# Kernel optimization log

Hardware: AMD Instinct MI355X
Metric: run time of the kernel (lower is better)

## Reference

```python
import jax, jax.numpy as jnp
import numpy as np
from jax import lax

B, T, C = 8, 1025, 512
HEADS = 8
CACHE = 256          # int(dim * cache_ratio)
CLS = 1
L = 256              # gr_cache memory length
H = W = 32           # sqrt(T - CLS)
EPS = 1e-5


def setup_inputs() -> dict:
    key = jax.random.key(0)
    ks = jax.random.split(key, 40)
    def w(k, shape, scale=0.02):
        return jax.random.normal(k, shape, dtype=jnp.float32) * scale
    inp = {}
    inp['x'] = jax.random.normal(ks[0], (B, T, C), dtype=jnp.float32)
    inp['gr_cache'] = jax.random.normal(ks[1], (1, L, CACHE), dtype=jnp.float32)
    # self-attention (dim=512) params, weights stored (in, out)
    inp['Wq1'] = w(ks[2], (C, C)); inp['bq1'] = jnp.zeros((C,), jnp.float32)
    inp['Wk1'] = w(ks[3], (C, C)); inp['bk1'] = jnp.zeros((C,), jnp.float32)
    inp['Wv1'] = w(ks[4], (C, C)); inp['bv1'] = jnp.zeros((C,), jnp.float32)
    inp['Wo1'] = w(ks[5], (C, C)); inp['bo1'] = jnp.zeros((C,), jnp.float32)
    # memory attention (dim=cache_dim=256) params
    inp['Wq2'] = w(ks[6], (CACHE, CACHE)); inp['bq2'] = jnp.zeros((CACHE,), jnp.float32)
    inp['Wk2'] = w(ks[7], (CACHE, CACHE)); inp['bk2'] = jnp.zeros((CACHE,), jnp.float32)
    inp['Wv2'] = w(ks[8], (CACHE, CACHE)); inp['bv2'] = jnp.zeros((CACHE,), jnp.float32)
    inp['Wo2'] = w(ks[9], (CACHE, CACHE)); inp['bo2'] = jnp.zeros((CACHE,), jnp.float32)
    # GRU-style gate linears: in = 2*cache_dim, out = cache_dim
    inp['Wr'] = w(ks[10], (2 * CACHE, CACHE)); inp['br'] = jnp.zeros((CACHE,), jnp.float32)
    inp['Wz'] = w(ks[11], (2 * CACHE, CACHE)); inp['bz'] = jnp.zeros((CACHE,), jnp.float32)
    inp['Wa'] = w(ks[12], (2 * CACHE, CACHE)); inp['ba'] = jnp.zeros((CACHE,), jnp.float32)
    # LayerNorm(cache_dim)
    inp['gamma'] = jnp.ones((CACHE,), jnp.float32)
    inp['beta'] = jnp.zeros((CACHE,), jnp.float32)
    # per-head gate logits, init to -1 as in the module
    inp['lam'] = jnp.full((HEADS,), -1.0, dtype=jnp.float32)
    # grouped conv pos-emb: Conv2d(512, 512, k=3, groups=CACHE) -> (O=512, I/g=2, 3, 3)
    inp['conv_w'] = w(ks[13], (C, C // CACHE, 3, 3))
    inp['conv_b'] = jnp.zeros((C,), jnp.float32)
    return inp


def _mha(q_in, kv_in, Wq, bq, Wk, bk, Wv, bv, Wo, bo):
    Bq, Tq, D = q_in.shape
    Tk = kv_in.shape[1]
    dh = D // HEADS
    q = (q_in @ Wq + bq).reshape(Bq, Tq, HEADS, dh)
    k = (kv_in @ Wk + bk).reshape(Bq, Tk, HEADS, dh)
    v = (kv_in @ Wv + bv).reshape(Bq, Tk, HEADS, dh)
    s = jnp.einsum('bqhd,bkhd->bhqk', q, k) * (1.0 / np.sqrt(dh)).astype(np.float32)
    a = jax.nn.softmax(s, axis=-1)
    o = jnp.einsum('bhqk,bkhd->bqhd', a, v).reshape(Bq, Tq, D)
    return o @ Wo + bo


def reference(x, gr_cache, Wq1, bq1, Wk1, bk1, Wv1, bv1, Wo1, bo1,
              Wq2, bq2, Wk2, bk2, Wv2, bv2, Wo2, bo2,
              Wr, br, Wz, bz, Wa, ba, gamma, beta, lam, conv_w, conv_b):
    B_, T_, C_ = x.shape
    # ---- spatial positional embedding (faithful to torch view->permute quirk) ----
    tok = x[:, CLS:, :].reshape(B_, H, W, C_).transpose(0, 3, 1, 2)   # (B, C, H, W)
    pos = lax.conv_general_dilated(tok, conv_w, (1, 1), 'SAME',
                                   feature_group_count=CACHE,
                                   dimension_numbers=('NCHW', 'OIHW', 'NCHW'))
    pos = pos + conv_b[None, :, None, None]
    pos = pos.reshape(B_, C_, T_ - CLS).transpose(0, 2, 1)            # (B, T-1, C)
    pos = jnp.concatenate([jnp.zeros((B_, CLS, C_), pos.dtype), pos], axis=1)
    # ---- self attention ----
    x_self = _mha(x, x, Wq1, bq1, Wk1, bk1, Wv1, bv1, Wo1, bo1)       # (B, T, C)
    x_self_h = x_self.reshape(B_, T_, HEADS, C_ // HEADS)
    # ---- GRU-style gated cache update ----
    gr = jnp.broadcast_to(gr_cache, (B_, L, CACHE))
    x_summary = x_self[:, :, :CACHE]
    idx = (jnp.arange(L) * T_) // L                                   # nearest interpolate T -> L
    x_summary = x_summary[:, idx, :]                                  # (B, L, CACHE)
    cat = jnp.concatenate([gr, x_summary], axis=-1)
    reset = jax.nn.sigmoid(cat @ Wr + br)
    z = jax.nn.sigmoid(cat @ Wz + bz)
    cat2 = jnp.concatenate([reset * gr, x_summary], axis=-1)
    add = jax.nn.gelu(cat2 @ Wa + ba, approximate=False)
    mu = add.mean(-1, keepdims=True)
    var = ((add - mu) ** 2).mean(-1, keepdims=True)
    add = (add - mu) / jnp.sqrt(var + EPS) * gamma + beta             # LayerNorm
    gr_new = z * add + (1.0 - z) * gr
    # ---- memory attention on first cache_dim channels ----
    x_mem = _mha(x[:, :, :CACHE], gr_new, Wq2, bq2, Wk2, bk2, Wv2, bv2, Wo2, bo2)
    x_mem = x_mem.reshape(B_, T_, HEADS, CACHE // HEADS)
    # ---- per-head alpha blend with zero-padded mem branch ----
    alpha = jax.nn.sigmoid(lam).reshape(1, 1, HEADS, 1)
    pad = jnp.zeros((B_, T_, HEADS, (C_ - CACHE) // HEADS), x.dtype)
    out = (alpha * jnp.concatenate([x_mem, pad], axis=-1)
           + (1.0 - alpha) * x_self_h).reshape(B_, T_, C_) + pos
    return out
```

## Files before the change

kernel.cpp:

```cpp
#include <hip/hip_runtime.h>
#include <math.h>

typedef unsigned short u16;
typedef unsigned int u32;
typedef __attribute__((ext_vector_type(8))) short short8;
typedef __attribute__((ext_vector_type(4))) short short4v;
typedef __attribute__((ext_vector_type(4))) float f32x4;

constexpr int Bc = 8;
constexpr int Tt = 1025;
constexpr int Cc = 512;
constexpr int Hn = 8;
constexpr int CA = 256;
constexpr int Ll = 256;

#if __has_builtin(__builtin_amdgcn_exp2f)
#define EXP2F __builtin_amdgcn_exp2f
#else
#define EXP2F exp2f
#endif

__device__ __forceinline__ u16 f2bf(float f) {
  u32 u = __builtin_bit_cast(u32, f);
  u = (u + 0x7FFFu + ((u >> 16) & 1u)) >> 16;
  return (u16)u;
}
__device__ __forceinline__ u32 pack2f(float lo, float hi) {
  const u32 a = __builtin_bit_cast(u32, hi) + 0x8000u;
  const u32 b = __builtin_bit_cast(u32, lo) + 0x8000u;
  return __builtin_amdgcn_perm(a, b, 0x07060302u);
}

struct WC { const float* s; u16* d; int sN; int sK; int kshift; int tot; };
struct WCP { WC w[11]; };

__global__ void wcast_k(WCP p) {
  const WC a = p.w[blockIdx.y];
  const int kmask = (1 << a.kshift) - 1;
  for (int idx = blockIdx.x * 256 + threadIdx.x; idx < a.tot; idx += gridDim.x * 256) {
    const int k = idx & kmask;
    const int n = idx >> a.kshift;
    a.d[idx] = (k < a.sK) ? f2bf(a.s[(size_t)k * a.sN + n]) : (u16)0;
  }
}

enum { EP_NONE = 0, EP_SIGMOID = 1, EP_GELU = 2 };

struct GemmEpi {
  const float* bias[4];
  int start[4];
  float scale[4];
  int nreg;
};

template <int AF32, int OUTBF, int ACT>
__global__ __launch_bounds__(256) void gemm_mfma(
    const void* __restrict__ Av, int lda,
    const u16* __restrict__ Wt,
    GemmEpi epi,
    void* __restrict__ Cout,
    int M, int N, int K)
{
  __shared__ u16 As[128][32];
  __shared__ u16 Bs[128][32];
  const int tid = threadIdx.x;
  const int m0 = blockIdx.y * 128, n0 = blockIdx.x * 128;
  const int ln = tid & 15, quad = (tid >> 4) & 3, wv = tid >> 6;
  const int wm = (wv & 1) * 64, wn = (wv >> 1) * 64;
  const int sr = tid >> 1;
  const int sk = (tid & 1) * 16;

  f32x4 zf = {0.f, 0.f, 0.f, 0.f};
  f32x4 acc[4][4];
  #pragma unroll
  for (int i = 0; i < 4; i++)
    #pragma unroll
    for (int j = 0; j < 4; j++) acc[i][j] = zf;

  const short8 z8 = {0, 0, 0, 0, 0, 0, 0, 0};

  for (int k0 = 0; k0 < K; k0 += 32) {
    const int gm = m0 + sr;
    short8 a0 = z8, a1 = z8;
    if (gm < M) {
      if (AF32) {
        const float* p = (const float*)Av + (size_t)gm * lda + k0 + sk;
        const float4 f0 = *(const float4*)(p + 0);
        const float4 f1 = *(const float4*)(p + 4);
        const float4 f2 = *(const float4*)(p + 8);
        const float4 f3 = *(const float4*)(p + 12);
        ((u32*)&a0)[0] = pack2f(f0.x, f0.y);
        ((u32*)&a0)[1] = pack2f(f0.z, f0.w);
        ((u32*)&a0)[2] = pack2f(f1.x, f1.y);
        ((u32*)&a0)[3] = pack2f(f1.z, f1.w);
        ((u32*)&a1)[0] = pack2f(f2.x, f2.y);
        ((u32*)&a1)[1] = pack2f(f2.z, f2.w);
        ((u32*)&a1)[2] = pack2f(f3.x, f3.y);
        ((u32*)&a1)[3] = pack2f(f3.z, f3.w);
      } else {
        const u16* p = (const u16*)Av + (size_t)gm * lda + k0 + sk;
        a0 = *(const short8*)p;
        a1 = *(const short8*)(p + 8);
      }
    }
    *(short8*)&As[sr][sk] = a0;
    *(short8*)&As[sr][sk + 8] = a1;
    {
      const u16* q = Wt + (size_t)(n0 + sr) * K + k0 + sk;
      *(short8*)&Bs[sr][sk] = *(const short8*)q;
      *(short8*)&Bs[sr][sk + 8] = *(const short8*)(q + 8);
    }
    __syncthreads();

    short8 af[4], bf[4];
    #pragma unroll
    for (int i = 0; i < 4; i++) af[i] = *(const short8*)&As[wm + i * 16 + ln][quad * 8];
    #pragma unroll
    for (int j = 0; j < 4; j++) bf[j] = *(const short8*)&Bs[wn + j * 16 + ln][quad * 8];
    #pragma unroll
    for (int i = 0; i < 4; i++)
      #pragma unroll
      for (int j = 0; j < 4; j++)
        acc[i][j] = __builtin_amdgcn_mfma_f32_16x16x32_bf16(af[i], bf[j], acc[i][j], 0, 0, 0);
    __syncthreads();
  }

  int ri = 0;
  #pragma unroll
  for (int i = 1; i < 4; i++)
    if (i < epi.nreg && epi.start[i] <= n0) ri = i;
  const float* bp = epi.bias[ri] - epi.start[ri];
  const float sc = epi.scale[ri];

  float bj[4];
  #pragma unroll
  for (int j = 0; j < 4; j++) bj[j] = bp[n0 + wn + j * 16 + ln];

  #pragma unroll
  for (int i = 0; i < 4; i++) {
    #pragma unroll
    for (int r = 0; r < 4; r++) {
      const int gm = m0 + wm + i * 16 + quad * 4 + r;
      if (gm >= M) continue;
      #pragma unroll
      for (int j = 0; j < 4; j++) {
        float v = (acc[i][j][r] + bj[j]) * sc;
        if (ACT == EP_SIGMOID)   v = 1.f / (1.f + __expf(-v));
        else if (ACT == EP_GELU) v = 0.5f * v * (1.f + erff(v * 0.70710678118654752f));
        const size_t off = (size_t)gm * N + n0 + wn + j * 16 + ln;
        if (OUTBF) ((u16*)Cout)[off] = f2bf(v);
        else       ((float*)Cout)[off] = v;
      }
    }
  }
}

template <int DH>
__global__ __launch_bounds__(128) void attn_mfma(
    const u16* __restrict__ Qp, const u16* __restrict__ Kp,
    const u16* __restrict__ Vp, u16* __restrict__ Op,
    int Tq, int Tk, int qbs, int kbs, int obs, int qrs, int krs, int ors)
{
  constexpr int NC = DH / 32;
  constexpr int NM = DH / 16;

  __shared__ u16 Vt[2][DH * 32];
  __shared__ u16 Pb[2 * 32 * 32];

  const int b = blockIdx.y >> 3, h = blockIdx.y & 7;
  const int q0 = blockIdx.x * 64;
  const int tid = threadIdx.x;
  const int wv = tid >> 6;
  const int lane = tid & 63;
  const int ln = lane & 15, quad = lane >> 4;

  const u16* Qb = Qp + (size_t)b * qbs + h * DH;
  const u16* Kb = Kp + (size_t)b * kbs + h * DH;
  const u16* Vb = Vp + (size_t)b * kbs + h * DH;
  u16* Ob = Op + (size_t)b * obs + h * DH;

  const short8 z8 = {0, 0, 0, 0, 0, 0, 0, 0};
  const f32x4 zf = {0.f, 0.f, 0.f, 0.f};

  short8 qf[2][NC];
  #pragma unroll
  for (int qs = 0; qs < 2; qs++) {
    const int gq = q0 + wv * 32 + qs * 16 + ln;
    #pragma unroll
    for (int c = 0; c < NC; c++) {
      if (gq < Tq) qf[qs][c] = *(const short8*)(Qb + (size_t)gq * qrs + c * 32 + quad * 8);
      else         qf[qs][c] = z8;
    }
  }

  f32x4 oacc[2][NM];
  float lsum[2] = {0.f, 0.f};
  #pragma unroll
  for (int qs = 0; qs < 2; qs++)
    #pragma unroll
    for (int c = 0; c < NM; c++) oacc[qs][c] = zf;

  const int vd0 = (tid & 15) * (DH / 16);
  const int vk = (tid >> 4) * 4;
  const int gb = vk >> 3, off = vk & 7;

  const int nfull = Tk >> 5;
  const int nit = (Tk + 31) >> 5;
  const int tkm1 = Tk - 1;

  auto loadK = [&](int it, short8 (&kf)[2][NC]) {
    #pragma unroll
    for (int kc = 0; kc < 2; kc++)
      #pragma unroll
      for (int c = 0; c < NC; c++) {
        int row = (it << 5) + kc * 16 + ln;
        row = row < tkm1 ? row : tkm1;
        kf[kc][c] = *(const short8*)(Kb + (size_t)row * krs + c * 32 + quad * 8);
      }
  };
  auto loadV = [&](int it, short4v (&vr)[4]) {
    #pragma unroll
    for (int i2 = 0; i2 < 4; i2++) {
      int gk = (it << 5) + vk + i2;
      gk = gk < tkm1 ? gk : tkm1;
      short4v t = {0, 0, 0, 0};
      if (DH == 64) {
        t = *(const short4v*)(Vb + (size_t)gk * krs + vd0);
      } else {
        ushort2 u = *(const ushort2*)(Vb + (size_t)gk * krs + vd0);
        t[0] = (short)u.x; t[1] = (short)u.y;
      }
      vr[i2] = t;
    }
  };

  auto body = [&](int it, short8 (&kfC)[2][NC], short4v (&vrC)[4],
                  short8 (&kfN)[2][NC], short4v (&vrN)[4]) {
    const bool full = (it < nfull);
    u16* vt = &Vt[it & 1][0];
    const int k0 = it << 5;

    #pragma unroll
    for (int i = 0; i < DH / 16; i++) {
      const int d = vd0 + i;
      const int h2 = (d ^ (d >> 3)) & 3;
      short4v w = {vrC[0][i], vrC[1][i], vrC[2][i], vrC[3][i]};
      *(short4v*)&vt[d * 32 + ((gb ^ h2) << 3) + off] = w;
    }
    if (it + 1 < nit) { loadK(it + 1, kfN); loadV(it + 1, vrN); }
    __syncthreads();

    #pragma unroll
    for (int qs = 0; qs < 2; qs++) {
      #pragma unroll
      for (int kc = 0; kc < 2; kc++) {
        f32x4 s = zf;
        #pragma unroll
        for (int c = 0; c < NC; c++)
          s = __builtin_amdgcn_mfma_f32_16x16x32_bf16(kfC[kc][c], qf[qs][c], s, 0, 0, 0);
        float p0, p1, p2, p3;
        if (full) {
          p0 = EXP2F(s[0]); p1 = EXP2F(s[1]); p2 = EXP2F(s[2]); p3 = EXP2F(s[3]);
        } else {
          const int kb = k0 + kc * 16 + quad * 4;
          p0 = (kb + 0 < Tk) ? EXP2F(s[0]) : 0.f;
          p1 = (kb + 1 < Tk) ? EXP2F(s[1]) : 0.f;
          p2 = (kb + 2 < Tk) ? EXP2F(s[2]) : 0.f;
          p3 = (kb + 3 < Tk) ? EXP2F(s[3]) : 0.f;
        }
        lsum[qs] += (p0 + p1) + (p2 + p3);
        short4v pw;
        ((u32*)&pw)[0] = pack2f(p0, p1);
        ((u32*)&pw)[1] = pack2f(p2, p3);
        const int q = qs * 16 + ln;
        const int g = ((kc * 2 + (quad >> 1)) ^ (ln & 3)) & 3;
        *(short4v*)&Pb[wv * 1024 + q * 32 + (g << 3) + (quad & 1) * 4] = pw;
      }
    }

    short8 pf2[2];
    #pragma unroll
    for (int qs = 0; qs < 2; qs++) {
      const int q = qs * 16 + ln;
      const int g = quad ^ (ln & 3);
      pf2[qs] = *(const short8*)&Pb[wv * 1024 + q * 32 + g * 8];
    }
    #pragma unroll
    for (int c = 0; c < NM; c++) {
      const int d = c * 16 + ln;
      const int g = quad ^ ((d ^ (d >> 3)) & 3);
      const short8 vf = *(const short8*)&vt[d * 32 + g * 8];
      #pragma unroll
      for (int qs = 0; qs < 2; qs++)
        oacc[qs][c] = __builtin_amdgcn_mfma_f32_16x16x32_bf16(pf2[qs], vf, oacc[qs][c], 0, 0, 0);
    }
  };

  short8 kfA[2][NC], kfB[2][NC];
  short4v vrA[4], vrB[4];
  loadK(0, kfA);
  loadV(0, vrA);

  int it = 0;
  for (; it + 1 < nit; it += 2) {
    body(it, kfA, vrA, kfB, vrB);
    body(it + 1, kfB, vrB, kfA, vrA);
  }
  if (it < nit) body(it, kfA, vrA, kfB, vrB);

  float lq[2];
  #pragma unroll
  for (int qs = 0; qs < 2; qs++) {
    float t = lsum[qs];
    t += __shfl_xor(t, 16);
    t += __shfl_xor(t, 32);
    lq[qs] = t;
  }
  #pragma unroll
  for (int qs = 0; qs < 2; qs++) {
    #pragma unroll
    for (int r = 0; r < 4; r++) {
      const float linv = 1.f / __shfl(lq[qs], quad * 4 + r);
      const int gq = q0 + wv * 32 + qs * 16 + quad * 4 + r;
      if (gq >= Tq) continue;
      #pragma unroll
      for (int c = 0; c < NM; c++)
        Ob[(size_t)gq * ors + c * 16 + ln] = f2bf(oacc[qs][c][r] * linv);
    }
  }
}

__global__ __launch_bounds__(256) void conv_combine(
    const float* __restrict__ x, const float* __restrict__ cw,
    const float* __restrict__ cb, const float* __restrict__ x_self,
    const float* __restrict__ x_mem, const float* __restrict__ lam,
    float* __restrict__ out)
{
  const int bh = blockIdx.x;
  const int b = bh >> 5, hh = bh & 31;
  const int c = (blockIdx.y << 8) + threadIdx.x;
  const int ci = c & ~1;
  const int dd = c & 63;
  const int h8 = c >> 6;
  const float alpha = 1.f / (1.f + __expf(-lam[h8]));
  const float bias = cb[c];

  float wgt[2][9];
  #pragma unroll
  for (int ch = 0; ch < 2; ch++)
    #pragma unroll
    for (int k = 0; k < 9; k++) wgt[ch][k] = cw[c * 18 + ch * 9 + k];

  const float* xrow[3];
  bool rv[3];
  #pragma unroll
  for (int r = 0; r < 3; r++) {
    const int h2 = hh + r - 1;
    rv[r] = (unsigned)h2 < 32u;
    xrow[r] = x + ((size_t)(b * Tt) + 1 + h2 * 32) * Cc + ci;
  }

  float2 win[3][3];
  #pragma unroll
  for (int r = 0; r < 3; r++) {
    win[r][0] = make_float2(0.f, 0.f);
    win[r][1] = rv[r] ? *(const float2*)(xrow[r]) : make_float2(0.f, 0.f);
  }

  const size_t bT = (size_t)b * Tt;
  for (int w = 0; w < 32; w++) {
    #pragma unroll
    for (int r = 0; r < 3; r++)
      win[r][2] = (rv[r] && w + 1 < 32) ? *(const float2*)(xrow[r] + (w + 1) * Cc)
                                        : make_float2(0.f, 0.f);
    float pos = bias;
    #pragma unroll
    for (int r = 0; r < 3; r++)
      #pragma unroll
      for (int col = 0; col < 3; col++) {
        pos += win[r][col].x * wgt[0][r * 3 + col];
        pos += win[r][col].y * wgt[1][r * 3 + col];
      }
    const size_t bt = bT + 1 + hh * 32 + w;
    const float mem = (dd < 32) ? x_mem[bt * 256 + h8 * 32 + dd] : 0.f;
    out[bt * 512 + c] = pos + alpha * mem + (1.f - alpha) * x_self[bt * 512 + c];
    #pragma unroll
    for (int r = 0; r < 3; r++) { win[r][0] = win[r][1]; win[r][1] = win[r][2]; }
  }

  if (hh == 0) {
    const float mem = (dd < 32) ? x_mem[bT * 256 + h8 * 32 + dd] : 0.f;
    out[bT * 512 + c] = alpha * mem + (1.f - alpha) * x_self[bT * 512 + c];
  }
}

__global__ void build_cat(const float* __restrict__ gr_cache,
                          const float* __restrict__ x_self,
                          u16* __restrict__ cat)
{
  const int idx = blockIdx.x * 256 + threadIdx.x;
  if (idx >= Bc * Ll * 512) return;
  const int k = idx & 511;
  const int bi = idx >> 9;
  const int i = bi & 255;
  const int b = bi >> 8;
  float v;
  if (k < 256) v = gr_cache[i * 256 + k];
  else         v = x_self[((size_t)(b * Tt + 4 * i)) * Cc + (k - 256)];
  cat[idx] = f2bf(v);
}

__global__ void build_cat2(const float* __restrict__ gr_cache,
                           const float* __restrict__ rzg,
                           u16* __restrict__ cat)
{
  const int idx = blockIdx.x * 256 + threadIdx.x;
  if (idx >= Bc * Ll * 256) return;
  const int k = idx & 255;
  const int bi = idx >> 8;
  const int i = bi & 255;
  cat[(size_t)bi * 512 + k] = f2bf(gr_cache[i * 256 + k] * rzg[(size_t)bi * 512 + k]);
}

__device__ inline float block_sum256(float v, float* red)
{
  #pragma unroll
  for (int o = 32; o >= 1; o >>= 1) v += __shfl_down(v, o);
  const int wid = threadIdx.x >> 6;
  if ((threadIdx.x & 63) == 0) red[wid] = v;
  __syncthreads();
  const float t = red[0] + red[1] + red[2] + red[3];
  __syncthreads();
  return t;
}

__global__ __launch_bounds__(256) void ln_gate(
    const float* __restrict__ add_raw, const float* __restrict__ rzg,
    const float* __restrict__ gr_cache, const float* __restrict__ gamma,
    const float* __restrict__ beta, u16* __restrict__ gr_new)
{
  __shared__ float red[4];
  const int bi = blockIdx.x;
  const int i = bi & 255;
  const int c = threadIdx.x;
  const float v = add_raw[(size_t)bi * 256 + c];
  const float mu = block_sum256(v, red) * (1.f / 256.f);
  const float dv = v - mu;
  const float var = block_sum256(dv * dv, red) * (1.f / 256.f);
  const float nrm = dv * rsqrtf(var + 1e-5f) * gamma[c] + beta[c];
  const float zz = rzg[(size_t)bi * 512 + 256 + c];
  gr_new[(size_t)bi * 256 + c] = f2bf(zz * nrm + (1.f - zz) * gr_cache[i * 256 + c]);
}

extern "C" void kernel_launch(void* const* d_in, const int* in_sizes, int n_in,
                              void* d_out, int out_size, void* d_ws, size_t ws_size,
                              hipStream_t stream)
{
  const float* x        = (const float*)d_in[0];
  const float* gr_cache = (const float*)d_in[1];
  const float* Wq1 = (const float*)d_in[2];  const float* bq1 = (const float*)d_in[3];
  const float* Wk1 = (const float*)d_in[4];  const float* bk1 = (const float*)d_in[5];
  const float* Wv1 = (const float*)d_in[6];  const float* bv1 = (const float*)d_in[7];
  const float* Wo1 = (const float*)d_in[8];  const float* bo1 = (const float*)d_in[9];
  const float* Wq2 = (const float*)d_in[10]; const float* bq2 = (const float*)d_in[11];
  const float* Wk2 = (const float*)d_in[12]; const float* bk2 = (const float*)d_in[13];
  const float* Wv2 = (const float*)d_in[14]; const float* bv2 = (const float*)d_in[15];
  const float* Wo2 = (const float*)d_in[16]; const float* bo2 = (const float*)d_in[17];
  const float* Wr  = (const float*)d_in[18]; const float* br  = (const float*)d_in[19];
  const float* Wz  = (const float*)d_in[20]; const float* bz  = (const float*)d_in[21];
  const float* Wa  = (const float*)d_in[22]; const float* ba  = (const float*)d_in[23];
  const float* gamma = (const float*)d_in[24];
  const float* beta  = (const float*)d_in[25];
  const float* lam   = (const float*)d_in[26];
  const float* conv_w = (const float*)d_in[27];
  const float* conv_b = (const float*)d_in[28];
  float* out = (float*)d_out;

  const int M1 = Bc * Tt;
  const int M2 = Bc * Ll;
  const size_t BLA = (size_t)Bc * Ll * CA;
  const size_t BL2 = (size_t)Bc * Ll * 512;

  char* W = (char*)d_ws;
  u16*   qkvq  = (u16*)(W + 0);
  u16*   att1  = (u16*)(W + 29388800);
  u16*   att2  = (u16*)(W + 29388800);
  float* x_self= (float*)(W + 37785600);
  u16*   cat   = (u16*)(W + 54579200);
  float* rzg   = (float*)(W + 56676352);
  float* addr_ = (float*)(W + 60870656);
  float* x_mem = (float*)(W + 54579200);
  u16*   gr_new= (u16*)(W + 62976000);
  u16*   k2v2  = (u16*)(W + 64024576);
  u16*   wtb   = (u16*)(W + 66121728);

  u16* megaW = wtb;
  u16* o1W   = wtb + 917504;
  u16* rzW   = wtb + 1179648;
  u16* aW    = wtb + 1441792;
  u16* kvW   = wtb + 1572864;
  u16* o2W   = wtb + 1703936;

  const dim3 blk(256);

  {
    WCP p;
    p.w[0]  = {Wq1, megaW + 0,           512, 512, 9, 512 * 512};
    p.w[1]  = {Wk1, megaW + 512 * 512,   512, 512, 9, 512 * 512};
    p.w[2]  = {Wv1, megaW + 1024 * 512,  512, 512, 9, 512 * 512};
    p.w[3]  = {Wq2, megaW + 1536 * 512,  256, 256, 9, 256 * 512};
    p.w[4]  = {Wo1, o1W,                 512, 512, 9, 512 * 512};
    p.w[5]  = {Wr,  rzW + 0,             256, 512, 9, 256 * 512};
    p.w[6]  = {Wz,  rzW + 256 * 512,     256, 512, 9, 256 * 512};
    p.w[7]  = {Wa,  aW,                  256, 512, 9, 256 * 512};
    p.w[8]  = {Wk2, kvW + 0,             256, 256, 8, 256 * 256};
    p.w[9]  = {Wv2, kvW + 256 * 256,     256, 256, 8, 256 * 256};
    p.w[10] = {Wo2, o2W,                 256, 256, 8, 256 * 256};
    wcast_k<<<dim3(64, 11), blk, 0, stream>>>(p);
  }

  const float sQ1 = 0.18033688011112042f;
  const float sQ2 = 0.25503490664918414f;

  {
    GemmEpi e;
    e.bias[0] = bq1; e.start[0] = 0;    e.scale[0] = sQ1;
    e.bias[1] = bk1; e.start[1] = 512;  e.scale[1] = 1.f;
    e.bias[2] = bv1; e.start[2] = 1024; e.scale[2] = 1.f;
    e.bias[3] = bq2; e.start[3] = 1536; e.scale[3] = sQ2;
    e.nreg = 4;
    gemm_mfma<1, 1, EP_NONE><<<dim3(14, 65), blk, 0, stream>>>(
        x, 512, megaW, e, qkvq, M1, 1792, 512);
  }

  attn_mfma<64><<<dim3(17, 64), dim3(128), 0, stream>>>(
      qkvq, qkvq + 512, qkvq + 1024, att1, Tt, Tt,
      Tt * 1792, Tt * 1792, Tt * 512, 1792, 1792, 512);

  {
    GemmEpi e; e.bias[0] = bo1; e.start[0] = 0; e.scale[0] = 1.f; e.nreg = 1;
    gemm_mfma<0, 0, EP_NONE><<<dim3(4, 65), blk, 0, stream>>>(
        att1, 512, o1W, e, x_self, M1, 512, 512);
  }

  build_cat<<<(int)((BL2 + 255) / 256), blk, 0, stream>>>(gr_cache, x_self, cat);
  {
    GemmEpi e;
    e.bias[0] = br; e.start[0] = 0;   e.scale[0] = 1.f;
    e.bias[1] = bz; e.start[1] = 256; e.scale[1] = 1.f;
    e.nreg = 2;
    gemm_mfma<0, 0, EP_SIGMOID><<<dim3(4, 16), blk, 0, stream>>>(
        cat, 512, rzW, e, rzg, M2, 512, 512);
  }
  build_cat2<<<(int)((BLA + 255) / 256), blk, 0, stream>>>(gr_cache, rzg, cat);
  {
    GemmEpi e; e.bias[0] = ba; e.start[0] = 0; e.scale[0] = 1.f; e.nreg = 1;
    gemm_mfma<0, 0, EP_GELU><<<dim3(2, 16), blk, 0, stream>>>(
        cat, 512, aW, e, addr_, M2, 256, 512);
  }
  ln_gate<<<M2, blk, 0, stream>>>(addr_, rzg, gr_cache, gamma, beta, gr_new);

  {
    GemmEpi e;
    e.bias[0] = bk2; e.start[0] = 0;   e.scale[0] = 1.f;
    e.bias[1] = bv2; e.start[1] = 256; e.scale[1] = 1.f;
    e.nreg = 2;
    gemm_mfma<0, 1, EP_NONE><<<dim3(4, 16), blk, 0, stream>>>(
        gr_new, 256, kvW, e, k2v2, M2, 512, 256);
  }

  attn_mfma<32><<<dim3(17, 64), dim3(128), 0, stream>>>(
      qkvq + 1536, k2v2, k2v2 + 256, att2, Tt, Ll,
      Tt * 1792, Ll * 512, Tt * 256, 1792, 512, 256);

  {
    GemmEpi e; e.bias[0] = bo2; e.start[0] = 0; e.scale[0] = 1.f; e.nreg = 1;
    gemm_mfma<0, 0, EP_NONE><<<dim3(2, 65), blk, 0, stream>>>(
        att2, 256, o2W, e, x_mem, M1, 256, 256);
  }

  conv_combine<<<dim3(Bc * 32, 2), blk, 0, stream>>>(x, conv_w, conv_b, x_self,
                                                     x_mem, lam, out);
}
```

Measured before the change: 370.4 us.

## Split attention key range across two wave pairs and combine in LDS

The attention kernel now launches 256 threads per block. Two pairs of waves each process half of the key/value iterations for the same 64 queries, then reduce their partial output accumulators and row sums through shared memory before normalising. This doubles the waves available per block to hide memory and MFMA latency, given the modest block count. The cost is extra LDS for per-pair V tiles, a combine step with two barriers, and block-wide barriers now shared by both pairs.

```diff
diff --git a/kernel.cpp b/kernel.cpp
--- a/kernel.cpp
+++ b/kernel.cpp
@@ -156,23 +156,31 @@
 }
 
 template <int DH>
-__global__ __launch_bounds__(128) void attn_mfma(
+__global__ __launch_bounds__(256) void attn_mfma(
     const u16* __restrict__ Qp, const u16* __restrict__ Kp,
     const u16* __restrict__ Vp, u16* __restrict__ Op,
     int Tq, int Tk, int qbs, int kbs, int obs, int qrs, int krs, int ors)
 {
   constexpr int NC = DH / 32;
   constexpr int NM = DH / 16;
-
-  __shared__ u16 Vt[2][DH * 32];
-  __shared__ u16 Pb[2 * 32 * 32];
+  constexpr int VTE = 2 * DH * 32;
+  constexpr int PAY = 2 * NM * 4 + 2;
+  constexpr int PSTR = PAY | 1;
+
+  __shared__ __align__(16) char smem[2 * VTE * 2 + 4 * 1024 * 2];
+  static_assert(128 * PSTR * 4 <= 2 * VTE * 2 + 4 * 1024 * 2, "combine fits");
+  u16* const VtP = (u16*)smem;
+  u16* const PbP = (u16*)(smem + 2 * VTE * 2);
 
   const int b = blockIdx.y >> 3, h = blockIdx.y & 7;
   const int q0 = blockIdx.x * 64;
   const int tid = threadIdx.x;
   const int wv = tid >> 6;
+  const int pair = wv >> 1;
+  const int wvp = wv & 1;
   const int lane = tid & 63;
   const int ln = lane & 15, quad = lane >> 4;
+  const int lt = tid & 127;
 
   const u16* Qb = Qp + (size_t)b * qbs + h * DH;
   const u16* Kb = Kp + (size_t)b * kbs + h * DH;
@@ -185,7 +193,7 @@
   short8 qf[2][NC];
   #pragma unroll
   for (int qs = 0; qs < 2; qs++) {
-    const int gq = q0 + wv * 32 + qs * 16 + ln;
+    const int gq = q0 + wvp * 32 + qs * 16 + ln;
     #pragma unroll
     for (int c = 0; c < NC; c++) {
       if (gq < Tq) qf[qs][c] = *(const short8*)(Qb + (size_t)gq * qrs + c * 32 + quad * 8);
@@ -200,13 +208,16 @@
     #pragma unroll
     for (int c = 0; c < NM; c++) oacc[qs][c] = zf;
 
-  const int vd0 = (tid & 15) * (DH / 16);
-  const int vk = (tid >> 4) * 4;
+  const int vd0 = (lt & 15) * (DH / 16);
+  const int vk = (lt >> 4) * 4;
   const int gb = vk >> 3, off = vk & 7;
 
   const int nfull = Tk >> 5;
   const int nit = (Tk + 31) >> 5;
   const int tkm1 = Tk - 1;
+  const int np = (nit + 1) >> 1;
+  const int it0 = pair * np;
+  const int itE = it0 + np;
 
   auto loadK = [&](int it, short8 (&kf)[2][NC]) {
     #pragma unroll
@@ -237,7 +248,7 @@
   auto body = [&](int it, short8 (&kfC)[2][NC], short4v (&vrC)[4],
                   short8 (&kfN)[2][NC], short4v (&vrN)[4]) {
     const bool full = (it < nfull);
-    u16* vt = &Vt[it & 1][0];
+    u16* vt = VtP + pair * VTE + (it & 1) * (DH * 32);
     const int k0 = it << 5;
 
     #pragma unroll
@@ -247,7 +258,7 @@
       short4v w = {vrC[0][i], vrC[1][i], vrC[2][i], vrC[3][i]};
       *(short4v*)&vt[d * 32 + ((gb ^ h2) << 3) + off] = w;
     }
-    if (it + 1 < nit) { loadK(it + 1, kfN); loadV(it + 1, vrN); }
+    if (it + 1 < itE) { loadK(it + 1, kfN); loadV(it + 1, vrN); }
     __syncthreads();
 
     #pragma unroll
@@ -274,7 +285,7 @@
         ((u32*)&pw)[1] = pack2f(p2, p3);
         const int q = qs * 16 + ln;
         const int g = ((kc * 2 + (quad >> 1)) ^ (ln & 3)) & 3;
-        *(short4v*)&Pb[wv * 1024 + q * 32 + (g << 3) + (quad & 1) * 4] = pw;
+        *(short4v*)&PbP[wv * 1024 + q * 32 + (g << 3) + (quad & 1) * 4] = pw;
       }
     }
 
@@ -283,7 +294,7 @@
     for (int qs = 0; qs < 2; qs++) {
       const int q = qs * 16 + ln;
       const int g = quad ^ (ln & 3);
-      pf2[qs] = *(const short8*)&Pb[wv * 1024 + q * 32 + g * 8];
+      pf2[qs] = *(const short8*)&PbP[wv * 1024 + q * 32 + g * 8];
     }
     #pragma unroll
     for (int c = 0; c < NM; c++) {
@@ -298,15 +309,44 @@
 
   short8 kfA[2][NC], kfB[2][NC];
   short4v vrA[4], vrB[4];
-  loadK(0, kfA);
-  loadV(0, vrA);
-
-  int it = 0;
-  for (; it + 1 < nit; it += 2) {
-    body(it, kfA, vrA, kfB, vrB);
-    body(it + 1, kfB, vrB, kfA, vrA);
-  }
-  if (it < nit) body(it, kfA, vrA, kfB, vrB);
+  loadK(it0, kfA);
+  loadV(it0, vrA);
+
+  int j = 0;
+  for (; j + 1 < np; j += 2) {
+    body(it0 + j, kfA, vrA, kfB, vrB);
+    body(it0 + j + 1, kfB, vrB, kfA, vrA);
+  }
+  if (j < np) body(it0 + j, kfA, vrA, kfB, vrB);
+
+  __syncthreads();
+  float* const cbuf = (float*)smem;
+  if (wv >= 2) {
+    float* dst = cbuf + ((wv - 2) * 64 + lane) * PSTR;
+    int idx = 0;
+    #pragma unroll
+    for (int qs = 0; qs < 2; qs++)
+      #pragma unroll
+      for (int c = 0; c < NM; c++)
+        #pragma unroll
+        for (int r = 0; r < 4; r++) dst[idx++] = oacc[qs][c][r];
+    dst[idx++] = lsum[0];
+    dst[idx]   = lsum[1];
+  }
+  __syncthreads();
+  if (wv >= 2) return;
+  {
+    const float* src = cbuf + (wv * 64 + lane) * PSTR;
+    int idx = 0;
+    #pragma unroll
+    for (int qs = 0; qs < 2; qs++)
+      #pragma unroll
+      for (int c = 0; c < NM; c++)
+        #pragma unroll
+        for (int r = 0; r < 4; r++) oacc[qs][c][r] += src[idx++];
+    lsum[0] += src[idx++];
+    lsum[1] += src[idx];
+  }
 
   float lq[2];
   #pragma unroll
@@ -321,7 +361,7 @@
     #pragma unroll
     for (int r = 0; r < 4; r++) {
       const float linv = 1.f / __shfl(lq[qs], quad * 4 + r);
-      const int gq = q0 + wv * 32 + qs * 16 + quad * 4 + r;
+      const int gq = q0 + wvp * 32 + qs * 16 + quad * 4 + r;
       if (gq >= Tq) continue;
       #pragma unroll
       for (int c = 0; c < NM; c++)
@@ -533,7 +573,7 @@
         x, 512, megaW, e, qkvq, M1, 1792, 512);
   }
 
-  attn_mfma<64><<<dim3(17, 64), dim3(128), 0, stream>>>(
+  attn_mfma<64><<<dim3(17, 64), dim3(256), 0, stream>>>(
       qkvq, qkvq + 512, qkvq + 1024, att1, Tt, Tt,
       Tt * 1792, Tt * 1792, Tt * 512, 1792, 1792, 512);
 
@@ -569,7 +609,7 @@
         gr_new, 256, kvW, e, k2v2, M2, 512, 256);
   }
 
-  attn_mfma<32><<<dim3(17, 64), dim3(128), 0, stream>>>(
+  attn_mfma<32><<<dim3(17, 64), dim3(256), 0, stream>>>(
       qkvq + 1536, k2v2, k2v2 + 256, att2, Tt, Ll,
       Tt * 1792, Ll * 512, Tt * 256, 1792, 512, 256);
 
```

Result: faster. 359.6 us (-2.9%).
